# Optimization experiments

Measured on AMD Instinct MI355X. Metric: run time of the kernel, lower is better.

## Reference

```python
import jax, jax.numpy as jnp
import numpy as np

N_POINTS = 1048576
LEVELS = 16
LOG2T = 19
TABLE_SIZE = 1 << LOG2T  # 524288
FEAT = 2
MIN_RES = 16.0
MAX_RES = 512.0


def setup_inputs() -> dict:
    key = jax.random.key(0)
    kx, kt = jax.random.split(key)
    bounding_box = jnp.array([[-1.5, -1.5, -1.5], [1.5, 1.5, 1.5]], dtype=jnp.float32)
    # sample mostly inside the box, a few points slightly outside to exercise clamp/keep_mask
    x = jax.random.uniform(kx, (N_POINTS, 3), dtype=jnp.float32, minval=-1.6, maxval=1.6)
    # torch init: uniform(-1e-4, 1e-4) per level embedding table
    tables = jax.random.uniform(kt, (LEVELS, TABLE_SIZE, FEAT), dtype=jnp.float32,
                                minval=-1e-4, maxval=1e-4)
    return {"x": x, "bounding_box": bounding_box, "tables": tables}


def _hash_encode(x, bounding_box, tables):
    min_b, max_b = bounding_box[0], bounding_box[1]  # [3]
    # keep_mask: point unchanged by clamping in every dim
    keep_mask = jnp.all((x >= min_b) & (x <= max_b), axis=-1)
    xc = jnp.clip(x, min_b, max_b)
    u = (xc - min_b) / (max_b - min_b)  # normalized to [0,1], [N,3]

    b = jnp.exp((jnp.log(MAX_RES) - jnp.log(MIN_RES)) / (LEVELS - 1))
    PI = jnp.array([1, 2654435761, 805459861], dtype=jnp.uint32)
    HASH_MASK = jnp.uint32(TABLE_SIZE - 1)
    # 8 corner offsets in (i,j,k) order matching the torch module
    offs = jnp.array([[i, j, k] for i in (0, 1) for j in (0, 1) for k in (0, 1)],
                     dtype=jnp.int32)  # [8,3]

    outs = []
    for level in range(LEVELS):
        Nl = jnp.floor(MIN_RES * b ** level)            # scalar resolution
        box_size = (max_b - min_b) / Nl                 # [3]
        grid = jnp.floor(u * Nl).astype(jnp.int32)      # [N,3] min-corner grid coords
        vmin = grid.astype(x.dtype) * box_size + min_b  # [N,3]
        vmax = vmin + box_size                          # [N,3]
        corners = (grid[:, None, :] + offs[None, :, :]).astype(jnp.uint32)  # [N,8,3]
        # spatial hash: xor of coord*prime, wrap-around in uint32 matches low bits of torch int64
        h = (corners[..., 0] * PI[0]) ^ (corners[..., 1] * PI[1]) ^ (corners[..., 2] * PI[2])
        idx = (h & HASH_MASK).astype(jnp.int32)         # [N,8]
        emb = tables[level][idx]                        # gather -> [N,8,F]
        # trilinear interpolation; note: uses ORIGINAL (unclamped) x, as in the torch code
        w = (x - vmin) / (vmax - vmin)                  # [N,3]
        wx, wy, wz = w[:, 0:1], w[:, 1:2], w[:, 2:3]
        c00 = emb[:, 0] * (1 - wx) + emb[:, 4] * wx
        c01 = emb[:, 1] * (1 - wx) + emb[:, 5] * wx
        c10 = emb[:, 2] * (1 - wx) + emb[:, 6] * wx
        c11 = emb[:, 3] * (1 - wx) + emb[:, 7] * wx
        c0 = c00 * (1 - wy) + c10 * wy
        c1 = c01 * (1 - wy) + c11 * wy
        outs.append(c0 * (1 - wz) + c1 * wz)            # [N,F]
    return jnp.concatenate(outs, axis=-1), keep_mask    # [N, L*F], [N]


def reference(x, bounding_box, tables):
    return _hash_encode(x, bounding_box, tables)
```

## Files before the change

### kernel.cpp

```cpp
#include <hip/hip_runtime.h>

#define NPTS   1048576
#define NLEV   16
#define TSIZE  (1u << 19)
#define HMASK  (TSIZE - 1u)

__device__ __constant__ float NLF_TAB[16] = {
    16.f, 20.f, 25.f, 32.f, 40.f, 50.f, 64.f, 80.f,
    101.f, 128.f, 161.f, 203.f, 256.f, 322.f, 406.f, 512.f};

__device__ __forceinline__ void level_lerp(
    float x0, float x1, float x2, float u0, float u1, float u2,
    float Nl, const float2* __restrict__ tab, float* r0, float* r1)
{
#pragma clang fp contract(off)
    const float mn = -1.5f, rng = 3.0f;
    const float box = rng / Nl;

    int g0 = (int)floorf(u0 * Nl);
    int g1 = (int)floorf(u1 * Nl);
    int g2 = (int)floorf(u2 * Nl);

    float vmin0 = (float)g0 * box + mn;
    float vmin1 = (float)g1 * box + mn;
    float vmin2 = (float)g2 * box + mn;

    float den0 = (vmin0 + box) - vmin0;
    float den1 = (vmin1 + box) - vmin1;
    float den2 = (vmin2 + box) - vmin2;

    float wx = (x0 - vmin0) / den0;
    float wy = (x1 - vmin1) / den1;
    float wz = (x2 - vmin2) / den2;

    unsigned hx0 = (unsigned)g0;
    unsigned hx1 = (unsigned)(g0 + 1);
    unsigned hy0 = (unsigned)g1       * 2654435761u;
    unsigned hy1 = (unsigned)(g1 + 1) * 2654435761u;
    unsigned hz0 = (unsigned)g2       * 805459861u;
    unsigned hz1 = (unsigned)(g2 + 1) * 805459861u;

    float2 e000 = tab[(hx0 ^ hy0 ^ hz0) & HMASK];
    float2 e001 = tab[(hx0 ^ hy0 ^ hz1) & HMASK];
    float2 e010 = tab[(hx0 ^ hy1 ^ hz0) & HMASK];
    float2 e011 = tab[(hx0 ^ hy1 ^ hz1) & HMASK];
    float2 e100 = tab[(hx1 ^ hy0 ^ hz0) & HMASK];
    float2 e101 = tab[(hx1 ^ hy0 ^ hz1) & HMASK];
    float2 e110 = tab[(hx1 ^ hy1 ^ hz0) & HMASK];
    float2 e111 = tab[(hx1 ^ hy1 ^ hz1) & HMASK];

    float omx = 1.0f - wx, omy = 1.0f - wy, omz = 1.0f - wz;
    {
        float c00 = e000.x * omx + e100.x * wx;
        float c01 = e001.x * omx + e101.x * wx;
        float c10 = e010.x * omx + e110.x * wx;
        float c11 = e011.x * omx + e111.x * wx;
        float c0  = c00 * omy + c10 * wy;
        float c1  = c01 * omy + c11 * wy;
        *r0 = c0 * omz + c1 * wz;
    }
    {
        float c00 = e000.y * omx + e100.y * wx;
        float c01 = e001.y * omx + e101.y * wx;
        float c10 = e010.y * omx + e110.y * wx;
        float c11 = e011.y * omx + e111.y * wx;
        float c0  = c00 * omy + c10 * wy;
        float c1  = c01 * omy + c11 * wy;
        *r1 = c0 * omz + c1 * wz;
    }
}

__global__ __launch_bounds__(256)
void coarse_kernel(const float* __restrict__ xin,
                   const float* __restrict__ tables,
                   float* __restrict__ out)
{
#pragma clang fp contract(off)
    int p = blockIdx.x * 256 + threadIdx.x;
    if (p >= NPTS) return;

    float x0 = xin[3 * p + 0];
    float x1 = xin[3 * p + 1];
    float x2 = xin[3 * p + 2];

    const float mn = -1.5f, mx = 1.5f, rng = 3.0f;

    float keep = (x0 >= mn && x0 <= mx &&
                  x1 >= mn && x1 <= mx &&
                  x2 >= mn && x2 <= mx) ? 1.0f : 0.0f;

    float u0 = (fminf(fmaxf(x0, mn), mx) - mn) / rng;
    float u1 = (fminf(fmaxf(x1, mn), mx) - mn) / rng;
    float u2 = (fminf(fmaxf(x2, mn), mx) - mn) / rng;

    float res[16];
#pragma unroll
    for (int l = 0; l < 8; ++l) {
        const float2* tab = (const float2*)tables + (size_t)l * TSIZE;
        level_lerp(x0, x1, x2, u0, u1, u2, NLF_TAB[l], tab,
                   &res[2 * l], &res[2 * l + 1]);
    }

    float4* orow = (float4*)(out + (size_t)p * 32);
#pragma unroll
    for (int i = 0; i < 4; ++i)
        orow[i] = make_float4(res[4 * i + 0], res[4 * i + 1],
                              res[4 * i + 2], res[4 * i + 3]);

    out[(size_t)NPTS * 32 + p] = keep;
}

template<int L>
__global__ __launch_bounds__(256)
void fine_kernel(const float* __restrict__ xin,
                 const float* __restrict__ tables,
                 float* __restrict__ out)
{
#pragma clang fp contract(off)
    int p = blockIdx.x * 256 + threadIdx.x;
    if (p >= NPTS) return;

    float x0 = xin[3 * p + 0];
    float x1 = xin[3 * p + 1];
    float x2 = xin[3 * p + 2];

    const float mn = -1.5f, mx = 1.5f, rng = 3.0f;

    float u0 = (fminf(fmaxf(x0, mn), mx) - mn) / rng;
    float u1 = (fminf(fmaxf(x1, mn), mx) - mn) / rng;
    float u2 = (fminf(fmaxf(x2, mn), mx) - mn) / rng;

    const float2* tab = (const float2*)tables + (size_t)L * TSIZE;
    float r0, r1;
    level_lerp(x0, x1, x2, u0, u1, u2, NLF_TAB[L], tab, &r0, &r1);

    *(float2*)(out + (size_t)p * 32 + 2 * L) = make_float2(r0, r1);
}

extern "C" void kernel_launch(void* const* d_in, const int* in_sizes, int n_in,
                              void* d_out, int out_size, void* d_ws, size_t ws_size,
                              hipStream_t stream) {
    const float* x      = (const float*)d_in[0];
    const float* tables = (const float*)d_in[2];
    float* out = (float*)d_out;

    int n = in_sizes[0] / 3;
    int blocks = (n + 255) / 256;

    coarse_kernel<<<blocks, 256, 0, stream>>>(x, tables, out);
    fine_kernel< 8><<<blocks, 256, 0, stream>>>(x, tables, out);
    fine_kernel< 9><<<blocks, 256, 0, stream>>>(x, tables, out);
    fine_kernel<10><<<blocks, 256, 0, stream>>>(x, tables, out);
    fine_kernel<11><<<blocks, 256, 0, stream>>>(x, tables, out);
    fine_kernel<12><<<blocks, 256, 0, stream>>>(x, tables, out);
    fine_kernel<13><<<blocks, 256, 0, stream>>>(x, tables, out);
    fine_kernel<14><<<blocks, 256, 0, stream>>>(x, tables, out);
    fine_kernel<15><<<blocks, 256, 0, stream>>>(x, tables, out);
}
```

Before: 542.3 us.

## Morton-sort points into buckets so coarse and mid level gathers run spatially coherent

Adds a histogram, scan and scatter pass that bins points into 32^3 Morton buckets in workspace, storing the original index and packed coordinates with the keep flag. Levels 0 to 9 are then computed in sorted order so neighbouring threads hit nearby hash table entries, and levels 8 and 9 are merged into a single kernel. Fine levels keep the original-order per-level kernels. This adds several extra passes, heavy atomics, and scattered output writes in exchange for better cache locality on the gathers.

```diff
diff --git a/kernel.cpp b/kernel.cpp
--- a/kernel.cpp
+++ b/kernel.cpp
@@ -4,10 +4,34 @@
 #define NLEV   16
 #define TSIZE  (1u << 19)
 #define HMASK  (TSIZE - 1u)
+#define NBUCK  32768
 
 __device__ __constant__ float NLF_TAB[16] = {
     16.f, 20.f, 25.f, 32.f, 40.f, 50.f, 64.f, 80.f,
     101.f, 128.f, 161.f, 203.f, 256.f, 322.f, 406.f, 512.f};
+
+__device__ __forceinline__ unsigned spread5(unsigned x) {
+    x &= 0x1F;
+    x = (x | (x << 8)) & 0x100F;
+    x = (x | (x << 4)) & 0x10C3;
+    x = (x | (x << 2)) & 0x1249;
+    return x;
+}
+
+__device__ __forceinline__ unsigned morton_key(float u0, float u1, float u2) {
+    unsigned k0 = min(31u, (unsigned)(u0 * 32.0f));
+    unsigned k1 = min(31u, (unsigned)(u1 * 32.0f));
+    unsigned k2 = min(31u, (unsigned)(u2 * 32.0f));
+    return (spread5(k0) << 2) | (spread5(k1) << 1) | spread5(k2);
+}
+
+__device__ __forceinline__ void uvw(float x0, float x1, float x2,
+                                    float* u0, float* u1, float* u2) {
+    const float mn = -1.5f, mx = 1.5f, rng = 3.0f;
+    *u0 = (fminf(fmaxf(x0, mn), mx) - mn) / rng;
+    *u1 = (fminf(fmaxf(x1, mn), mx) - mn) / rng;
+    *u2 = (fminf(fmaxf(x2, mn), mx) - mn) / rng;
+}
 
 __device__ __forceinline__ void level_lerp(
     float x0, float x1, float x2, float u0, float u1, float u2,
@@ -70,6 +94,135 @@
     }
 }
 
+
+__global__ __launch_bounds__(256)
+void hist_kernel(const float* __restrict__ xin, unsigned* __restrict__ hist)
+{
+    int p = blockIdx.x * 256 + threadIdx.x;
+    if (p >= NPTS) return;
+    float x0 = xin[3 * p], x1 = xin[3 * p + 1], x2 = xin[3 * p + 2];
+    float u0, u1, u2; uvw(x0, x1, x2, &u0, &u1, &u2);
+    atomicAdd(&hist[morton_key(u0, u1, u2)], 1u);
+}
+
+__global__ __launch_bounds__(1024)
+void scan_kernel(unsigned* __restrict__ hist, unsigned* __restrict__ cursor)
+{
+    __shared__ unsigned part[1024];
+    int t = threadIdx.x;
+    unsigned local[32];
+    unsigned s = 0;
+#pragma unroll
+    for (int i = 0; i < 32; ++i) { local[i] = hist[t * 32 + i]; s += local[i]; }
+    part[t] = s;
+    __syncthreads();
+    for (int off = 1; off < 1024; off <<= 1) {
+        unsigned v = (t >= off) ? part[t - off] : 0;
+        __syncthreads();
+        part[t] += v;
+        __syncthreads();
+    }
+    unsigned base = (t == 0) ? 0u : part[t - 1];
+#pragma unroll
+    for (int i = 0; i < 32; ++i) {
+        cursor[t * 32 + i] = base;
+        base += local[i];
+    }
+}
+
+__global__ __launch_bounds__(256)
+void scatter_kernel(const float* __restrict__ xin,
+                    unsigned* __restrict__ cursor,
+                    unsigned* __restrict__ sidx,
+                    float4* __restrict__ sx4)
+{
+    int p = blockIdx.x * 256 + threadIdx.x;
+    if (p >= NPTS) return;
+    float x0 = xin[3 * p], x1 = xin[3 * p + 1], x2 = xin[3 * p + 2];
+    float u0, u1, u2; uvw(x0, x1, x2, &u0, &u1, &u2);
+    const float mn = -1.5f, mx = 1.5f;
+    float keep = (x0 >= mn && x0 <= mx &&
+                  x1 >= mn && x1 <= mx &&
+                  x2 >= mn && x2 <= mx) ? 1.0f : 0.0f;
+    unsigned pos = atomicAdd(&cursor[morton_key(u0, u1, u2)], 1u);
+    sidx[pos] = (unsigned)p;
+    sx4[pos] = make_float4(x0, x1, x2, keep);
+}
+
+
+__global__ __launch_bounds__(256)
+void coarse_sorted(const unsigned* __restrict__ sidx,
+                   const float4* __restrict__ sx4,
+                   const float* __restrict__ tables,
+                   float* __restrict__ out)
+{
+#pragma clang fp contract(off)
+    int s = blockIdx.x * 256 + threadIdx.x;
+    if (s >= NPTS) return;
+    unsigned p = sidx[s];
+    float4 xv = sx4[s];
+    float u0, u1, u2; uvw(xv.x, xv.y, xv.z, &u0, &u1, &u2);
+
+    float res[16];
+#pragma unroll
+    for (int l = 0; l < 8; ++l) {
+        const float2* tab = (const float2*)tables + (size_t)l * TSIZE;
+        level_lerp(xv.x, xv.y, xv.z, u0, u1, u2, NLF_TAB[l], tab,
+                   &res[2 * l], &res[2 * l + 1]);
+    }
+
+    float4* orow = (float4*)(out + (size_t)p * 32);
+#pragma unroll
+    for (int i = 0; i < 4; ++i)
+        orow[i] = make_float4(res[4 * i + 0], res[4 * i + 1],
+                              res[4 * i + 2], res[4 * i + 3]);
+    out[(size_t)NPTS * 32 + p] = xv.w;
+}
+
+__global__ __launch_bounds__(256)
+void mid_sorted(const unsigned* __restrict__ sidx,
+                const float4* __restrict__ sx4,
+                const float* __restrict__ tables,
+                float* __restrict__ out)
+{
+#pragma clang fp contract(off)
+    int s = blockIdx.x * 256 + threadIdx.x;
+    if (s >= NPTS) return;
+    unsigned p = sidx[s];
+    float4 xv = sx4[s];
+    float u0, u1, u2; uvw(xv.x, xv.y, xv.z, &u0, &u1, &u2);
+
+    float r[4];
+    {
+        const float2* tab = (const float2*)tables + (size_t)8 * TSIZE;
+        level_lerp(xv.x, xv.y, xv.z, u0, u1, u2, NLF_TAB[8], tab, &r[0], &r[1]);
+    }
+    {
+        const float2* tab = (const float2*)tables + (size_t)9 * TSIZE;
+        level_lerp(xv.x, xv.y, xv.z, u0, u1, u2, NLF_TAB[9], tab, &r[2], &r[3]);
+    }
+    *(float4*)(out + (size_t)p * 32 + 16) = make_float4(r[0], r[1], r[2], r[3]);
+}
+
+template<int L>
+__global__ __launch_bounds__(256)
+void fine_kernel(const float* __restrict__ xin,
+                 const float* __restrict__ tables,
+                 float* __restrict__ out)
+{
+#pragma clang fp contract(off)
+    int p = blockIdx.x * 256 + threadIdx.x;
+    if (p >= NPTS) return;
+    float x0 = xin[3 * p], x1 = xin[3 * p + 1], x2 = xin[3 * p + 2];
+    float u0, u1, u2; uvw(x0, x1, x2, &u0, &u1, &u2);
+
+    const float2* tab = (const float2*)tables + (size_t)L * TSIZE;
+    float r0, r1;
+    level_lerp(x0, x1, x2, u0, u1, u2, NLF_TAB[L], tab, &r0, &r1);
+    *(float2*)(out + (size_t)p * 32 + 2 * L) = make_float2(r0, r1);
+}
+
+
 __global__ __launch_bounds__(256)
 void coarse_kernel(const float* __restrict__ xin,
                    const float* __restrict__ tables,
@@ -78,20 +231,12 @@
 #pragma clang fp contract(off)
     int p = blockIdx.x * 256 + threadIdx.x;
     if (p >= NPTS) return;
-
-    float x0 = xin[3 * p + 0];
-    float x1 = xin[3 * p + 1];
-    float x2 = xin[3 * p + 2];
-
-    const float mn = -1.5f, mx = 1.5f, rng = 3.0f;
-
+    float x0 = xin[3 * p], x1 = xin[3 * p + 1], x2 = xin[3 * p + 2];
+    const float mn = -1.5f, mx = 1.5f;
     float keep = (x0 >= mn && x0 <= mx &&
                   x1 >= mn && x1 <= mx &&
                   x2 >= mn && x2 <= mx) ? 1.0f : 0.0f;
-
-    float u0 = (fminf(fmaxf(x0, mn), mx) - mn) / rng;
-    float u1 = (fminf(fmaxf(x1, mn), mx) - mn) / rng;
-    float u2 = (fminf(fmaxf(x2, mn), mx) - mn) / rng;
+    float u0, u1, u2; uvw(x0, x1, x2, &u0, &u1, &u2);
 
     float res[16];
 #pragma unroll
@@ -100,41 +245,12 @@
         level_lerp(x0, x1, x2, u0, u1, u2, NLF_TAB[l], tab,
                    &res[2 * l], &res[2 * l + 1]);
     }
-
     float4* orow = (float4*)(out + (size_t)p * 32);
 #pragma unroll
     for (int i = 0; i < 4; ++i)
         orow[i] = make_float4(res[4 * i + 0], res[4 * i + 1],
                               res[4 * i + 2], res[4 * i + 3]);
-
     out[(size_t)NPTS * 32 + p] = keep;
-}
-
-template<int L>
-__global__ __launch_bounds__(256)
-void fine_kernel(const float* __restrict__ xin,
-                 const float* __restrict__ tables,
-                 float* __restrict__ out)
-{
-#pragma clang fp contract(off)
-    int p = blockIdx.x * 256 + threadIdx.x;
-    if (p >= NPTS) return;
-
-    float x0 = xin[3 * p + 0];
-    float x1 = xin[3 * p + 1];
-    float x2 = xin[3 * p + 2];
-
-    const float mn = -1.5f, mx = 1.5f, rng = 3.0f;
-
-    float u0 = (fminf(fmaxf(x0, mn), mx) - mn) / rng;
-    float u1 = (fminf(fmaxf(x1, mn), mx) - mn) / rng;
-    float u2 = (fminf(fmaxf(x2, mn), mx) - mn) / rng;
-
-    const float2* tab = (const float2*)tables + (size_t)L * TSIZE;
-    float r0, r1;
-    level_lerp(x0, x1, x2, u0, u1, u2, NLF_TAB[L], tab, &r0, &r1);
-
-    *(float2*)(out + (size_t)p * 32 + 2 * L) = make_float2(r0, r1);
 }
 
 extern "C" void kernel_launch(void* const* d_in, const int* in_sizes, int n_in,
@@ -147,13 +263,38 @@
     int n = in_sizes[0] / 3;
     int blocks = (n + 255) / 256;
 
-    coarse_kernel<<<blocks, 256, 0, stream>>>(x, tables, out);
-    fine_kernel< 8><<<blocks, 256, 0, stream>>>(x, tables, out);
-    fine_kernel< 9><<<blocks, 256, 0, stream>>>(x, tables, out);
-    fine_kernel<10><<<blocks, 256, 0, stream>>>(x, tables, out);
-    fine_kernel<11><<<blocks, 256, 0, stream>>>(x, tables, out);
-    fine_kernel<12><<<blocks, 256, 0, stream>>>(x, tables, out);
-    fine_kernel<13><<<blocks, 256, 0, stream>>>(x, tables, out);
-    fine_kernel<14><<<blocks, 256, 0, stream>>>(x, tables, out);
-    fine_kernel<15><<<blocks, 256, 0, stream>>>(x, tables, out);
-}
+    const size_t HIST_B   = (size_t)NBUCK * 4;
+    const size_t SIDX_OFF = 131072;
+    const size_t SX4_OFF  = SIDX_OFF + (size_t)NPTS * 4;
+    const size_t NEEDED   = SX4_OFF + (size_t)NPTS * 16;
+
+    if (ws_size >= NEEDED) {
+        unsigned* hist = (unsigned*)d_ws;
+        unsigned* sidx = (unsigned*)((char*)d_ws + SIDX_OFF);
+        float4*   sx4  = (float4*)((char*)d_ws + SX4_OFF);
+
+        hipMemsetAsync(hist, 0, HIST_B, stream);
+        hist_kernel<<<blocks, 256, 0, stream>>>(x, hist);
+        scan_kernel<<<1, 1024, 0, stream>>>(hist, hist);
+        scatter_kernel<<<blocks, 256, 0, stream>>>(x, hist, sidx, sx4);
+
+        coarse_sorted<<<blocks, 256, 0, stream>>>(sidx, sx4, tables, out);
+        mid_sorted<<<blocks, 256, 0, stream>>>(sidx, sx4, tables, out);
+        fine_kernel<10><<<blocks, 256, 0, stream>>>(x, tables, out);
+        fine_kernel<11><<<blocks, 256, 0, stream>>>(x, tables, out);
+        fine_kernel<12><<<blocks, 256, 0, stream>>>(x, tables, out);
+        fine_kernel<13><<<blocks, 256, 0, stream>>>(x, tables, out);
+        fine_kernel<14><<<blocks, 256, 0, stream>>>(x, tables, out);
+        fine_kernel<15><<<blocks, 256, 0, stream>>>(x, tables, out);
+    } else {
+        coarse_kernel<<<blocks, 256, 0, stream>>>(x, tables, out);
+        fine_kernel< 8><<<blocks, 256, 0, stream>>>(x, tables, out);
+        fine_kernel< 9><<<blocks, 256, 0, stream>>>(x, tables, out);
+        fine_kernel<10><<<blocks, 256, 0, stream>>>(x, tables, out);
+        fine_kernel<11><<<blocks, 256, 0, stream>>>(x, tables, out);
+        fine_kernel<12><<<blocks, 256, 0, stream>>>(x, tables, out);
+        fine_kernel<13><<<blocks, 256, 0, stream>>>(x, tables, out);
+        fine_kernel<14><<<blocks, 256, 0, stream>>>(x, tables, out);
+        fine_kernel<15><<<blocks, 256, 0, stream>>>(x, tables, out);
+    }
+}
```

After: 484.5 us. 1.12x faster.
